# Performance work log

Hardware: AMD Instinct MI355X
Metric: run time of the kernel (lower is better)

The kernel has to match this reference:

```python
import jax, jax.numpy as jnp
import numpy as np

B, P, D, C = 1024, 4, 512, 128  # batch, parts, feat_dim, num_classes


def setup_inputs() -> dict:
    key = jax.random.key(0)
    k1, k2 = jax.random.split(key)
    # scale 0.05 keeps dot products O(1) so exp() stays in fp32 range
    inputs = jax.random.normal(k1, (B, P, D), dtype=jnp.float32) * 0.05
    targets = jax.random.randint(k2, (B,), 0, C, dtype=jnp.int64)
    return {"inputs": inputs, "targets": targets}


def _npairs_loss(inputs, targets):
    b, p, d = inputs.shape
    n = b * p
    X = inputs.reshape(n, d)
    t = jnp.repeat(targets, p)              # (n,) class label per row
    parts = jnp.tile(jnp.arange(p), b)      # (n,) part id per row
    prod = X @ X.T                          # (n, n) similarities

    sc = t[:, None] == t[None, :]           # same class
    sp = parts[:, None] == parts[None, :]   # same attention part
    s_sadc = (~sc) & sp
    s_dasc = sc & (~sp)
    s_dadc = (~sc) & (~sp)

    e_pos = jnp.exp(prod)                   # exp(neg) terms
    e_neg = jnp.exp(-prod)                  # exp(-pos) terms

    def group_loss(pos_mask, neg_mask):
        # sum_i sum_{j in pos_i} log(1 + sum_{k in neg_i} exp(prod[i,k] - prod[i,j]))
        # = sum log1p(S_i * exp(-prod[i,j])) with S_i = sum_{k in neg_i} exp(prod[i,k])
        S = jnp.sum(jnp.where(neg_mask, e_pos, 0.0), axis=1)        # (n,)
        terms = jnp.where(pos_mask, jnp.log1p(S[:, None] * e_neg), 0.0)
        return jnp.sum(terms)

    loss_sadc = group_loss(s_sadc, s_dadc)
    loss_dasc = group_loss(s_dasc, s_dadc)
    # NOTE: original returns loss_sadc twice and never uses loss_sasc (bug kept for fidelity)
    return (loss_sadc + loss_sadc + loss_dasc) / n


def reference(inputs, targets):
    return _npairs_loss(inputs, targets)
```

## Files before the change

### kernel.cpp

```cpp
#include <hip/hip_runtime.h>
#include <stdint.h>

#define GLOBAL_AS __attribute__((address_space(1)))
#define LDS_AS    __attribute__((address_space(3)))

typedef __attribute__((ext_vector_type(8))) __bf16 bf16x8;
typedef __attribute__((ext_vector_type(4))) float  f32x4;

static_assert(sizeof(bf16x8) == 16, "bf16x8 must be 16B");

constexpr int N  = 4096;
constexpr int DK = 512;


__global__ void k_convert(const float* __restrict__ X, __bf16* __restrict__ Xb,
                          const int* __restrict__ tbuf, int* __restrict__ cls) {
    if (blockIdx.x == 1024) {
        __shared__ int is64;
        const int t = threadIdx.x;
        if (t == 0) is64 = 1;
        __syncthreads();
        if (tbuf[4 * t + 1] != 0 || tbuf[4 * t + 3] != 0) is64 = 0;
        __syncthreads();
        const int f = is64;
#pragma unroll
        for (int q = 0; q < 4; ++q) {
            const int ti = 4 * t + q;
            const int v = tbuf[f ? 2 * ti : ti];
            cls[4 * ti + 0] = v; cls[4 * ti + 1] = v;
            cls[4 * ti + 2] = v; cls[4 * ti + 3] = v;
        }
        return;
    }
    int idx = blockIdx.x * blockDim.x + threadIdx.x;
    const float4* s = (const float4*)X;
    float4 a = s[2 * idx + 0];
    float4 b = s[2 * idx + 1];
    bf16x8 o;
    o[0] = (__bf16)a.x; o[1] = (__bf16)a.y; o[2] = (__bf16)a.z; o[3] = (__bf16)a.w;
    o[4] = (__bf16)b.x; o[5] = (__bf16)b.y; o[6] = (__bf16)b.z; o[7] = (__bf16)b.w;
    *(bf16x8*)(Xb + 8 * idx) = o;
}

__launch_bounds__(512, 4)
__global__ void k_main(const __bf16* __restrict__ Xb, const int* __restrict__ cls,
                       float* __restrict__ partials) {
    __shared__ __align__(16) __bf16 As[2][128 * 64];
    __shared__ __align__(16) __bf16 Bs[2][128 * 64];
    __shared__ float4 accR[4][128];
    __shared__ float4 accC[2][128];
    __shared__ int rowcls[128], colcls[128];

    const int tid  = threadIdx.x;
    const int lane = tid & 63;
    const int wid  = tid >> 6;
    const int wr   = wid >> 2;
    const int wc   = wid & 3;

    const int bid = (blockIdx.x & 7) * 66 + (blockIdx.x >> 3);
    int rt = (int)((sqrtf(8.0f * (float)bid + 1.0f) - 1.0f) * 0.5f);
    while (((rt + 1) * (rt + 2)) / 2 <= bid) ++rt;
    while ((rt * (rt + 1)) / 2 > bid) --rt;
    const int g  = bid - (rt * (rt + 1)) / 2;
    const int i0 = rt * 128;
    const int j0 = g * 128;
    const bool offdiag = (rt != g);

    if (tid < 128) {
        rowcls[tid] = cls[i0 + tid];
        colcls[tid] = cls[j0 + tid];
    }

    f32x4 acc[4][2] = {};

    const char* xb   = (const char*)Xb;
    const int   srow = tid >> 3;
    const int   skb  = ((tid & 7) ^ (srow & 7)) * 16;
    const int   ldst = wid * 1024;
    const int   rA   = lane & 15;
    const int   kgrp = lane >> 4;

#define STAGE(buf, kt)                                                                         \
    {                                                                                          \
        const size_t kb0 = (size_t)(kt) * 128;                                                 \
        char* AsB = (char*)(&As[(buf)][0]);                                                    \
        char* BsB = (char*)(&Bs[(buf)][0]);                                                    \
        _Pragma("unroll")                                                                      \
        for (int t = 0; t < 2; ++t) {                                                          \
            __builtin_amdgcn_global_load_lds(                                                  \
                (const GLOBAL_AS void*)(xb + (size_t)(i0 + t * 64 + srow) * 1024 + kb0 + skb), \
                (LDS_AS void*)(AsB + t * 8192 + ldst), 16, 0, 0);                              \
            __builtin_amdgcn_global_load_lds(                                                  \
                (const GLOBAL_AS void*)(xb + (size_t)(j0 + t * 64 + srow) * 1024 + kb0 + skb), \
                (LDS_AS void*)(BsB + t * 8192 + ldst), 16, 0, 0);                              \
        }                                                                                      \
    }

    STAGE(0, 0);
    __syncthreads();

    int cur = 0;
#pragma unroll
    for (int kt = 0; kt < DK / 64; ++kt) {
        if (kt < DK / 64 - 1) STAGE(cur ^ 1, kt + 1);
        const char* A_ = (const char*)(&As[cur][0]);
        const char* B_ = (const char*)(&Bs[cur][0]);
#pragma unroll
        for (int kk = 0; kk < 2; ++kk) {
            bf16x8 af[4];
            bf16x8 bg[2];
#pragma unroll
            for (int m = 0; m < 4; ++m) {
                const int r = wr * 64 + m * 16 + rA;
                af[m] = *(const bf16x8*)(A_ + r * 128 + (((kk * 4 + kgrp) ^ (r & 7)) * 16));
            }
#pragma unroll
            for (int n = 0; n < 2; ++n) {
                const int r = wc * 32 + n * 16 + rA;
                bg[n] = *(const bf16x8*)(B_ + r * 128 + (((kk * 4 + kgrp) ^ (r & 7)) * 16));
            }
#pragma unroll
            for (int m = 0; m < 4; ++m)
#pragma unroll
                for (int n = 0; n < 2; ++n)
                    acc[m][n] = __builtin_amdgcn_mfma_f32_16x16x32_bf16(bg[n], af[m],
                                                                        acc[m][n], 0, 0, 0);
        }
        if (kt < DK / 64 - 1) {
            __syncthreads();
            cur ^= 1;
        }
    }
#undef STAGE

    const int pi = rA & 3;
    int ci[4];
#pragma unroll
    for (int m = 0; m < 4; ++m) ci[m] = rowcls[wr * 64 + m * 16 + rA];

    float rS[4] = {0.f, 0.f, 0.f, 0.f};
    float rP[4] = {0.f, 0.f, 0.f, 0.f};
    float rE[4] = {0.f, 0.f, 0.f, 0.f};
    float rW[4] = {0.f, 0.f, 0.f, 0.f};

#pragma unroll
    for (int n = 0; n < 2; ++n) {
#pragma unroll
        for (int r = 0; r < 4; ++r) {
            const int cj = colcls[wc * 32 + n * 16 + kgrp * 4 + r];
            float cS = 0.f, cP = 0.f, cE = 0.f, cW = 0.f;
#pragma unroll
            for (int m = 0; m < 4; ++m) {
                const float p  = acc[m][n][r];
                const float ep = __expf(p);
                const bool sc = (ci[m] == cj);
                const bool sp = (pi == r);
                if (!sc && !sp) { rS[m] += ep; cS += ep; }
                const float w = (!sc && sp) ? 2.f : ((sc && !sp) ? 1.f : 0.f);
                rP[m] += w * p;  rE[m] += w * ep;  rW[m] += w;
                cP += w * p;     cE += w * ep;     cW += w;
            }
            if (offdiag) {
#pragma unroll
                for (int off = 1; off < 16; off <<= 1) {
                    cS += __shfl_xor(cS, off);
                    cP += __shfl_xor(cP, off);
                    cE += __shfl_xor(cE, off);
                    cW += __shfl_xor(cW, off);
                }
                if (rA == 0)
                    accC[wr][wc * 32 + n * 16 + kgrp * 4 + r] = make_float4(cS, cP, cE, cW);
            }
        }
    }
#pragma unroll
    for (int m = 0; m < 4; ++m) {
        float vS = rS[m], vP = rP[m], vE = rE[m], vW = rW[m];
        vS += __shfl_xor(vS, 16); vS += __shfl_xor(vS, 32);
        vP += __shfl_xor(vP, 16); vP += __shfl_xor(vP, 32);
        vE += __shfl_xor(vE, 16); vE += __shfl_xor(vE, 32);
        vW += __shfl_xor(vW, 16); vW += __shfl_xor(vW, 32);
        if (kgrp == 0) accR[wc][wr * 64 + m * 16 + rA] = make_float4(vS, vP, vE, vW);
    }

    __syncthreads();
    if (tid < 128) {
        float4 a0 = accR[0][tid], a1 = accR[1][tid], a2 = accR[2][tid], a3 = accR[3][tid];
        float4 o = make_float4(a0.x + a1.x + a2.x + a3.x, a0.y + a1.y + a2.y + a3.y,
                               a0.z + a1.z + a2.z + a3.z, a0.w + a1.w + a2.w + a3.w);
        ((float4*)partials)[(size_t)(i0 + tid) * 32 + g] = o;
        if (offdiag) {
            float4 c0 = accC[0][tid], c1 = accC[1][tid];
            float4 oc = make_float4(c0.x + c1.x, c0.y + c1.y, c0.z + c1.z, c0.w + c1.w);
            ((float4*)partials)[(size_t)(j0 + tid) * 32 + rt] = oc;
        }
    }
}

__global__ void k_rowloss(const float* __restrict__ partials, float* __restrict__ blockSums) {
    __shared__ float red[16];
    const int tid = threadIdx.x;
    const int sub = tid & 15;
    const int row = blockIdx.x * 16 + (tid >> 4);

    const float4* p = ((const float4*)partials) + (size_t)row * 32;
    float4 a = p[sub];
    float4 b = p[sub + 16];
    float S = a.x + b.x, P = a.y + b.y, E = a.z + b.z, W = a.w + b.w;
#pragma unroll
    for (int off = 1; off < 16; off <<= 1) {
        S += __shfl_xor(S, off);
        P += __shfl_xor(P, off);
        E += __shfl_xor(E, off);
        W += __shfl_xor(W, off);
    }
    if (sub == 0) red[tid >> 4] = W * logf(S) - P + E / S;
    __syncthreads();
    if (tid == 0) {
        float s = 0.f;
#pragma unroll
        for (int r = 0; r < 16; ++r) s += red[r];
        blockSums[blockIdx.x] = s;
    }
}

__global__ void k_final2(const float* __restrict__ blockSums, float* __restrict__ out) {
    const int t = threadIdx.x;
    float v = blockSums[t] + blockSums[t + 64] + blockSums[t + 128] + blockSums[t + 192];
#pragma unroll
    for (int off = 1; off < 64; off <<= 1) v += __shfl_xor(v, off);
    if (t == 0) out[0] = v / (float)N;
}

extern "C" void kernel_launch(void* const* d_in, const int* in_sizes, int n_in,
                              void* d_out, int out_size, void* d_ws, size_t ws_size,
                              hipStream_t stream) {
    const float* X = (const float*)d_in[0];
    const int*   T = (const int*)d_in[1];
    float* out = (float*)d_out;

    char* ws = (char*)d_ws;
    __bf16* Xb     = (__bf16*)ws;
    int*    cls    = (int*)(ws + (size_t)4 * 1024 * 1024);
    float*  parts  = (float*)(ws + (size_t)4 * 1024 * 1024 + 16 * 1024);
    float*  bsums  = (float*)ws;

    hipLaunchKernelGGL(k_convert, dim3(1025), dim3(256), 0, stream, X, Xb, T, cls);
    hipLaunchKernelGGL(k_main,    dim3(528),  dim3(512), 0, stream, Xb, cls, parts);
    hipLaunchKernelGGL(k_rowloss, dim3(256),  dim3(256), 0, stream, parts, bsums);
    hipLaunchKernelGGL(k_final2,  dim3(1),    dim3(64),  0, stream, bsums, out);
}
```

Measured before the change: 47.61 us.

## Use 128x64 triangular tiles with persistent work-stealing and triple-buffered LDS pipeline

Splits the lower-triangular Gram computation into finer 128x64 tiles (1056 tiles) processed by a persistent 1024-block grid. Idle blocks take more tiles through an atomic counter that k_convert initialises. The K loop now uses 3-stage LDS buffering with explicit vmcnt waits and a single barrier per step, and 256-thread blocks replace the 512-thread ones. The row-loss and final kernels are widened to read the new 96-slot partials layout and skip invalid slots. The aim is better load balance and less idle time from the tail and barriers, at the cost of atomic traffic and more partial slots to reduce.

```diff
diff --git a/kernel.cpp b/kernel.cpp
--- a/kernel.cpp
+++ b/kernel.cpp
@@ -11,14 +11,18 @@
 
 constexpr int N  = 4096;
 constexpr int DK = 512;
+constexpr int NTILE = 1056;
+constexpr int GRID_MAIN = 1024;
+constexpr int PW = 96;
 
 
 __global__ void k_convert(const float* __restrict__ X, __bf16* __restrict__ Xb,
-                          const int* __restrict__ tbuf, int* __restrict__ cls) {
+                          const int* __restrict__ tbuf, int* __restrict__ cls,
+                          int* __restrict__ ctr) {
     if (blockIdx.x == 1024) {
         __shared__ int is64;
         const int t = threadIdx.x;
-        if (t == 0) is64 = 1;
+        if (t == 0) { is64 = 1; ctr[0] = GRID_MAIN; }
         __syncthreads();
         if (tbuf[4 * t + 1] != 0 || tbuf[4 * t + 3] != 0) is64 = 0;
         __syncthreads();
@@ -42,82 +46,78 @@
     *(bf16x8*)(Xb + 8 * idx) = o;
 }
 
-__launch_bounds__(512, 4)
+__launch_bounds__(256, 4)
 __global__ void k_main(const __bf16* __restrict__ Xb, const int* __restrict__ cls,
-                       float* __restrict__ partials) {
-    __shared__ __align__(16) __bf16 As[2][128 * 64];
-    __shared__ __align__(16) __bf16 Bs[2][128 * 64];
-    __shared__ float4 accR[4][128];
-    __shared__ float4 accC[2][128];
-    __shared__ int rowcls[128], colcls[128];
+                       float* __restrict__ partials, int* __restrict__ ctr) {
+    __shared__ __align__(16) char smem[3][12288];
+    __shared__ int rowcls[128], colcls[64];
+    __shared__ int shsteal;
+    float4* accR = (float4*)&smem[0][0];
+    float4* accC = (float4*)&smem[1][0];
 
     const int tid  = threadIdx.x;
     const int lane = tid & 63;
     const int wid  = tid >> 6;
-    const int wr   = wid >> 2;
-    const int wc   = wid & 3;
-
-    const int bid = (blockIdx.x & 7) * 66 + (blockIdx.x >> 3);
-    int rt = (int)((sqrtf(8.0f * (float)bid + 1.0f) - 1.0f) * 0.5f);
-    while (((rt + 1) * (rt + 2)) / 2 <= bid) ++rt;
-    while ((rt * (rt + 1)) / 2 > bid) --rt;
-    const int g  = bid - (rt * (rt + 1)) / 2;
-    const int i0 = rt * 128;
-    const int j0 = g * 128;
-    const bool offdiag = (rt != g);
-
-    if (tid < 128) {
-        rowcls[tid] = cls[i0 + tid];
-        colcls[tid] = cls[j0 + tid];
-    }
-
-    f32x4 acc[4][2] = {};
-
-    const char* xb   = (const char*)Xb;
-    const int   srow = tid >> 3;
-    const int   skb  = ((tid & 7) ^ (srow & 7)) * 16;
-    const int   ldst = wid * 1024;
-    const int   rA   = lane & 15;
-    const int   kgrp = lane >> 4;
-
-#define STAGE(buf, kt)                                                                         \
-    {                                                                                          \
-        const size_t kb0 = (size_t)(kt) * 128;                                                 \
-        char* AsB = (char*)(&As[(buf)][0]);                                                    \
-        char* BsB = (char*)(&Bs[(buf)][0]);                                                    \
-        _Pragma("unroll")                                                                      \
-        for (int t = 0; t < 2; ++t) {                                                          \
-            __builtin_amdgcn_global_load_lds(                                                  \
-                (const GLOBAL_AS void*)(xb + (size_t)(i0 + t * 64 + srow) * 1024 + kb0 + skb), \
-                (LDS_AS void*)(AsB + t * 8192 + ldst), 16, 0, 0);                              \
-            __builtin_amdgcn_global_load_lds(                                                  \
-                (const GLOBAL_AS void*)(xb + (size_t)(j0 + t * 64 + srow) * 1024 + kb0 + skb), \
-                (LDS_AS void*)(BsB + t * 8192 + ldst), 16, 0, 0);                              \
-        }                                                                                      \
-    }
-
-    STAGE(0, 0);
-    __syncthreads();
-
-    int cur = 0;
-#pragma unroll
-    for (int kt = 0; kt < DK / 64; ++kt) {
-        if (kt < DK / 64 - 1) STAGE(cur ^ 1, kt + 1);
-        const char* A_ = (const char*)(&As[cur][0]);
-        const char* B_ = (const char*)(&Bs[cur][0]);
-#pragma unroll
-        for (int kk = 0; kk < 2; ++kk) {
-            bf16x8 af[4];
-            bf16x8 bg[2];
+    const int wr   = wid >> 1;
+    const int wc   = wid & 1;
+    const int rA   = lane & 15;
+    const int kgrp = lane >> 4;
+    const char* xb = (const char*)Xb;
+
+    int tile = (blockIdx.x & 7) * 132 + (blockIdx.x >> 3);
+
+    for (;;) {
+        int rt = (int)((sqrtf(4.0f * (float)tile + 1.0f) - 1.0f) * 0.5f);
+        while ((rt + 1) * (rt + 2) <= tile) ++rt;
+        while (rt * (rt + 1) > tile) --rt;
+        const int gc = tile - rt * (rt + 1);
+        const int i0 = rt * 128;
+        const int j0 = gc * 64;
+        const bool fullyBelow = (gc < 2 * rt);
+
+        if (tid < 128) rowcls[tid] = cls[i0 + tid];
+        else if (tid < 192) colcls[tid - 128] = cls[j0 + (tid - 128)];
+        __syncthreads();
+
+        f32x4 acc[4][2] = {};
+
+#define STAGE(bslot, kt)                                                                   \
+        {                                                                                  \
+            char* dst = &smem[(bslot)][0];                                                 \
+            const size_t kb = (size_t)(kt) * 64;                                           \
+            _Pragma("unroll")                                                              \
+            for (int q = 0; q < 3; ++q) {                                                  \
+                const int l    = q * 256 + tid;                                            \
+                const int prow = l >> 2;                                                   \
+                const int csrc = (l & 3) ^ ((prow >> 1) & 3);                              \
+                const int grow = (prow < 128) ? (i0 + prow) : (j0 + prow - 128);           \
+                __builtin_amdgcn_global_load_lds(                                          \
+                    (const GLOBAL_AS void*)(xb + (size_t)grow * 1024 + kb + csrc * 16),    \
+                    (LDS_AS void*)(dst + q * 4096 + wid * 1024), 16, 0, 0);                \
+            }                                                                              \
+        }
+
+        STAGE(0, 0);
+        STAGE(1, 1);
+
+#pragma unroll
+        for (int t = 0; t < 16; ++t) {
+            if (t < 15) { asm volatile("s_waitcnt vmcnt(3)" ::: "memory"); }
+            else        { asm volatile("s_waitcnt vmcnt(0)" ::: "memory"); }
+            __builtin_amdgcn_s_barrier();
+            asm volatile("" ::: "memory");
+            if (t + 2 < 16) STAGE((t + 2) % 3, t + 2);
+            const char* bp = &smem[t % 3][0];
+            bf16x8 af[4], bg[2];
 #pragma unroll
             for (int m = 0; m < 4; ++m) {
-                const int r = wr * 64 + m * 16 + rA;
-                af[m] = *(const bf16x8*)(A_ + r * 128 + (((kk * 4 + kgrp) ^ (r & 7)) * 16));
+                const int pr = wr * 64 + m * 16 + rA;
+                af[m] = *(const bf16x8*)(bp + pr * 64 + ((kgrp ^ ((pr >> 1) & 3)) << 4));
             }
 #pragma unroll
             for (int n = 0; n < 2; ++n) {
-                const int r = wc * 32 + n * 16 + rA;
-                bg[n] = *(const bf16x8*)(B_ + r * 128 + (((kk * 4 + kgrp) ^ (r & 7)) * 16));
+                const int pr = 128 + wc * 32 + n * 16 + rA;
+                bg[n] = *(const bf16x8*)(bp + pr * 64 + ((kgrp ^ ((pr >> 1) & 3)) << 4));
             }
 #pragma unroll
             for (int m = 0; m < 4; ++m)
@@ -126,110 +126,120 @@
                     acc[m][n] = __builtin_amdgcn_mfma_f32_16x16x32_bf16(bg[n], af[m],
                                                                         acc[m][n], 0, 0, 0);
         }
-        if (kt < DK / 64 - 1) {
-            __syncthreads();
-            cur ^= 1;
-        }
-    }
 #undef STAGE
 
-    const int pi = rA & 3;
-    int ci[4];
-#pragma unroll
-    for (int m = 0; m < 4; ++m) ci[m] = rowcls[wr * 64 + m * 16 + rA];
-
-    float rS[4] = {0.f, 0.f, 0.f, 0.f};
-    float rP[4] = {0.f, 0.f, 0.f, 0.f};
-    float rE[4] = {0.f, 0.f, 0.f, 0.f};
-    float rW[4] = {0.f, 0.f, 0.f, 0.f};
-
-#pragma unroll
-    for (int n = 0; n < 2; ++n) {
-#pragma unroll
-        for (int r = 0; r < 4; ++r) {
-            const int cj = colcls[wc * 32 + n * 16 + kgrp * 4 + r];
-            float cS = 0.f, cP = 0.f, cE = 0.f, cW = 0.f;
-#pragma unroll
-            for (int m = 0; m < 4; ++m) {
-                const float p  = acc[m][n][r];
-                const float ep = __expf(p);
-                const bool sc = (ci[m] == cj);
-                const bool sp = (pi == r);
-                if (!sc && !sp) { rS[m] += ep; cS += ep; }
-                const float w = (!sc && sp) ? 2.f : ((sc && !sp) ? 1.f : 0.f);
-                rP[m] += w * p;  rE[m] += w * ep;  rW[m] += w;
-                cP += w * p;     cE += w * ep;     cW += w;
+        __syncthreads();
+
+        const int pi = rA & 3;
+        int ci[4];
+#pragma unroll
+        for (int m = 0; m < 4; ++m) ci[m] = rowcls[wr * 64 + m * 16 + rA];
+        float rS[4] = {0.f, 0.f, 0.f, 0.f};
+        float rP[4] = {0.f, 0.f, 0.f, 0.f};
+        float rE[4] = {0.f, 0.f, 0.f, 0.f};
+        float rW[4] = {0.f, 0.f, 0.f, 0.f};
+
+#pragma unroll
+        for (int n = 0; n < 2; ++n) {
+#pragma unroll
+            for (int r = 0; r < 4; ++r) {
+                const int cj = colcls[wc * 32 + n * 16 + kgrp * 4 + r];
+                float cS = 0.f, cP = 0.f, cE = 0.f, cW = 0.f;
+#pragma unroll
+                for (int m = 0; m < 4; ++m) {
+                    const float p  = acc[m][n][r];
+                    const float ep = __expf(p);
+                    const bool sc = (ci[m] == cj);
+                    const bool sp = (pi == r);
+                    if (!sc && !sp) { rS[m] += ep; cS += ep; }
+                    const float w = (!sc && sp) ? 2.f : ((sc && !sp) ? 1.f : 0.f);
+                    rP[m] += w * p;  rE[m] += w * ep;  rW[m] += w;
+                    cP += w * p;     cE += w * ep;     cW += w;
+                }
+                if (fullyBelow) {
+#pragma unroll
+                    for (int off = 1; off < 16; off <<= 1) {
+                        cS += __shfl_xor(cS, off);
+                        cP += __shfl_xor(cP, off);
+                        cE += __shfl_xor(cE, off);
+                        cW += __shfl_xor(cW, off);
+                    }
+                    if (rA == 0)
+                        accC[wr * 64 + wc * 32 + n * 16 + kgrp * 4 + r] =
+                            make_float4(cS, cP, cE, cW);
+                }
             }
-            if (offdiag) {
-#pragma unroll
-                for (int off = 1; off < 16; off <<= 1) {
-                    cS += __shfl_xor(cS, off);
-                    cP += __shfl_xor(cP, off);
-                    cE += __shfl_xor(cE, off);
-                    cW += __shfl_xor(cW, off);
-                }
-                if (rA == 0)
-                    accC[wr][wc * 32 + n * 16 + kgrp * 4 + r] = make_float4(cS, cP, cE, cW);
-            }
-        }
-    }
-#pragma unroll
-    for (int m = 0; m < 4; ++m) {
-        float vS = rS[m], vP = rP[m], vE = rE[m], vW = rW[m];
-        vS += __shfl_xor(vS, 16); vS += __shfl_xor(vS, 32);
-        vP += __shfl_xor(vP, 16); vP += __shfl_xor(vP, 32);
-        vE += __shfl_xor(vE, 16); vE += __shfl_xor(vE, 32);
-        vW += __shfl_xor(vW, 16); vW += __shfl_xor(vW, 32);
-        if (kgrp == 0) accR[wc][wr * 64 + m * 16 + rA] = make_float4(vS, vP, vE, vW);
-    }
-
-    __syncthreads();
-    if (tid < 128) {
-        float4 a0 = accR[0][tid], a1 = accR[1][tid], a2 = accR[2][tid], a3 = accR[3][tid];
-        float4 o = make_float4(a0.x + a1.x + a2.x + a3.x, a0.y + a1.y + a2.y + a3.y,
-                               a0.z + a1.z + a2.z + a3.z, a0.w + a1.w + a2.w + a3.w);
-        ((float4*)partials)[(size_t)(i0 + tid) * 32 + g] = o;
-        if (offdiag) {
-            float4 c0 = accC[0][tid], c1 = accC[1][tid];
-            float4 oc = make_float4(c0.x + c1.x, c0.y + c1.y, c0.z + c1.z, c0.w + c1.w);
-            ((float4*)partials)[(size_t)(j0 + tid) * 32 + rt] = oc;
-        }
+        }
+#pragma unroll
+        for (int m = 0; m < 4; ++m) {
+            float vS = rS[m], vP = rP[m], vE = rE[m], vW = rW[m];
+            vS += __shfl_xor(vS, 16); vS += __shfl_xor(vS, 32);
+            vP += __shfl_xor(vP, 16); vP += __shfl_xor(vP, 32);
+            vE += __shfl_xor(vE, 16); vE += __shfl_xor(vE, 32);
+            vW += __shfl_xor(vW, 16); vW += __shfl_xor(vW, 32);
+            if (kgrp == 0) accR[wc * 128 + wr * 64 + m * 16 + rA] = make_float4(vS, vP, vE, vW);
+        }
+
+        __syncthreads();
+        if (tid < 128) {
+            float4 a0 = accR[tid], a1 = accR[128 + tid];
+            ((float4*)partials)[(size_t)(i0 + tid) * PW + gc] =
+                make_float4(a0.x + a1.x, a0.y + a1.y, a0.z + a1.z, a0.w + a1.w);
+        } else if (tid < 192 && fullyBelow) {
+            const int c = tid - 128;
+            float4 c0 = accC[c], c1 = accC[64 + c];
+            ((float4*)partials)[(size_t)(j0 + c) * PW + 64 + rt] =
+                make_float4(c0.x + c1.x, c0.y + c1.y, c0.z + c1.z, c0.w + c1.w);
+        }
+
+        if (tid == 0) shsteal = atomicAdd(ctr, 1);
+        __syncthreads();
+        const int t2 = shsteal;
+        if (t2 >= NTILE) break;
+        tile = (t2 & 7) * 132 + (t2 >> 3);
     }
 }
 
 __global__ void k_rowloss(const float* __restrict__ partials, float* __restrict__ blockSums) {
-    __shared__ float red[16];
+    __shared__ float red[4];
     const int tid = threadIdx.x;
-    const int sub = tid & 15;
-    const int row = blockIdx.x * 16 + (tid >> 4);
-
-    const float4* p = ((const float4*)partials) + (size_t)row * 32;
-    float4 a = p[sub];
-    float4 b = p[sub + 16];
-    float S = a.x + b.x, P = a.y + b.y, E = a.z + b.z, W = a.w + b.w;
-#pragma unroll
-    for (int off = 1; off < 16; off <<= 1) {
+    const int lane = tid & 63;
+    const int w = tid >> 6;
+    const int row = blockIdx.x * 4 + w;
+    const int dEnd   = 2 * (row >> 7) + 2;
+    const int mStart = ((row >> 6) + 2) >> 1;
+
+    const float4* p = (const float4*)partials + (size_t)row * PW;
+    float S = 0.f, P = 0.f, E = 0.f, W_ = 0.f;
+#pragma unroll
+    for (int s = lane; s < PW; s += 64) {
+        const bool valid = (s < 64) ? (s < dEnd) : ((s - 64) >= mStart);
+        if (valid) {
+            float4 v = p[s];
+            S += v.x; P += v.y; E += v.z; W_ += v.w;
+        }
+    }
+#pragma unroll
+    for (int off = 1; off < 64; off <<= 1) {
         S += __shfl_xor(S, off);
         P += __shfl_xor(P, off);
         E += __shfl_xor(E, off);
-        W += __shfl_xor(W, off);
-    }
-    if (sub == 0) red[tid >> 4] = W * logf(S) - P + E / S;
+        W_ += __shfl_xor(W_, off);
+    }
+    if (lane == 0) red[w] = W_ * logf(S) - P + E / S;
     __syncthreads();
-    if (tid == 0) {
-        float s = 0.f;
-#pragma unroll
-        for (int r = 0; r < 16; ++r) s += red[r];
-        blockSums[blockIdx.x] = s;
-    }
+    if (tid == 0) blockSums[blockIdx.x] = red[0] + red[1] + red[2] + red[3];
 }
 
 __global__ void k_final2(const float* __restrict__ blockSums, float* __restrict__ out) {
+    __shared__ float red[4];
     const int t = threadIdx.x;
-    float v = blockSums[t] + blockSums[t + 64] + blockSums[t + 128] + blockSums[t + 192];
+    float v = blockSums[t] + blockSums[t + 256] + blockSums[t + 512] + blockSums[t + 768];
 #pragma unroll
     for (int off = 1; off < 64; off <<= 1) v += __shfl_xor(v, off);
-    if (t == 0) out[0] = v / (float)N;
+    if ((t & 63) == 0) red[t >> 6] = v;
+    __syncthreads();
+    if (t == 0) out[0] = (red[0] + red[1] + red[2] + red[3]) / (float)N;
 }
 
 extern "C" void kernel_launch(void* const* d_in, const int* in_sizes, int n_in,
@@ -240,13 +250,14 @@
     float* out = (float*)d_out;
 
     char* ws = (char*)d_ws;
-    __bf16* Xb     = (__bf16*)ws;
-    int*    cls    = (int*)(ws + (size_t)4 * 1024 * 1024);
-    float*  parts  = (float*)(ws + (size_t)4 * 1024 * 1024 + 16 * 1024);
-    float*  bsums  = (float*)ws;
-
-    hipLaunchKernelGGL(k_convert, dim3(1025), dim3(256), 0, stream, X, Xb, T, cls);
-    hipLaunchKernelGGL(k_main,    dim3(528),  dim3(512), 0, stream, Xb, cls, parts);
-    hipLaunchKernelGGL(k_rowloss, dim3(256),  dim3(256), 0, stream, parts, bsums);
-    hipLaunchKernelGGL(k_final2,  dim3(1),    dim3(64),  0, stream, bsums, out);
-}
+    __bf16* Xb    = (__bf16*)ws;
+    int*    cls   = (int*)(ws + (size_t)4 * 1024 * 1024);
+    int*    ctr   = (int*)(ws + (size_t)4 * 1024 * 1024 + 16 * 1024);
+    float*  parts = (float*)(ws + (size_t)4 * 1024 * 1024 + 16 * 1024 + 256);
+    float*  bsums = (float*)ws;
+
+    hipLaunchKernelGGL(k_convert, dim3(1025), dim3(256), 0, stream, X, Xb, T, cls, ctr);
+    hipLaunchKernelGGL(k_main,    dim3(GRID_MAIN), dim3(256), 0, stream, Xb, cls, parts, ctr);
+    hipLaunchKernelGGL(k_rowloss, dim3(1024), dim3(256), 0, stream, parts, bsums);
+    hipLaunchKernelGGL(k_final2,  dim3(1),    dim3(256), 0, stream, bsums, out);
+}
```

New measurement: 54.62 us. +14.7%, slower.

## Drop LDS staging in tile GEMM; load MFMA fragments directly from global memory

Applied to the files above, without the earlier changes.

The main kernel no longer stages A/B tiles in LDS through double-buffered global_load_lds. Each wave now reads its bf16x8 fragments directly from global memory, relying on L1/L2 for reuse. The block shrinks from 8 to 4 waves, and each wave computes a larger 64x64 sub-tile (4x4 MFMA accumulators). This removes LDS traffic and the per-k-step barriers, but each fragment load is now a strided 16-byte global read with no explicit prefetch. It also raises register pressure and lowers the number of waves per block.

```diff
diff --git a/kernel.cpp b/kernel.cpp
--- a/kernel.cpp
+++ b/kernel.cpp
@@ -1,9 +1,6 @@
 #include <hip/hip_runtime.h>
 #include <stdint.h>
 
-#define GLOBAL_AS __attribute__((address_space(1)))
-#define LDS_AS    __attribute__((address_space(3)))
-
 typedef __attribute__((ext_vector_type(8))) __bf16 bf16x8;
 typedef __attribute__((ext_vector_type(4))) float  f32x4;
 
@@ -11,6 +8,8 @@
 
 constexpr int N  = 4096;
 constexpr int DK = 512;
+constexpr int NTILE = 528;
+constexpr int PW = 32;
 
 
 __global__ void k_convert(const float* __restrict__ X, __bf16* __restrict__ Xb,
@@ -42,20 +41,20 @@
     *(bf16x8*)(Xb + 8 * idx) = o;
 }
 
-__launch_bounds__(512, 4)
+__launch_bounds__(256, 3)
 __global__ void k_main(const __bf16* __restrict__ Xb, const int* __restrict__ cls,
                        float* __restrict__ partials) {
-    __shared__ __align__(16) __bf16 As[2][128 * 64];
-    __shared__ __align__(16) __bf16 Bs[2][128 * 64];
-    __shared__ float4 accR[4][128];
+    __shared__ float4 accR[2][128];
     __shared__ float4 accC[2][128];
     __shared__ int rowcls[128], colcls[128];
 
     const int tid  = threadIdx.x;
     const int lane = tid & 63;
     const int wid  = tid >> 6;
-    const int wr   = wid >> 2;
-    const int wc   = wid & 3;
+    const int wr   = wid >> 1;
+    const int wc   = wid & 1;
+    const int rA   = lane & 15;
+    const int kgrp = lane >> 4;
 
     const int bid = (blockIdx.x & 7) * 66 + (blockIdx.x >> 3);
     int rt = (int)((sqrtf(8.0f * (float)bid + 1.0f) - 1.0f) * 0.5f);
@@ -66,88 +65,50 @@
     const int j0 = g * 128;
     const bool offdiag = (rt != g);
 
-    if (tid < 128) {
-        rowcls[tid] = cls[i0 + tid];
-        colcls[tid] = cls[j0 + tid];
-    }
-
-    f32x4 acc[4][2] = {};
-
-    const char* xb   = (const char*)Xb;
-    const int   srow = tid >> 3;
-    const int   skb  = ((tid & 7) ^ (srow & 7)) * 16;
-    const int   ldst = wid * 1024;
-    const int   rA   = lane & 15;
-    const int   kgrp = lane >> 4;
-
-#define STAGE(buf, kt)                                                                         \
-    {                                                                                          \
-        const size_t kb0 = (size_t)(kt) * 128;                                                 \
-        char* AsB = (char*)(&As[(buf)][0]);                                                    \
-        char* BsB = (char*)(&Bs[(buf)][0]);                                                    \
-        _Pragma("unroll")                                                                      \
-        for (int t = 0; t < 2; ++t) {                                                          \
-            __builtin_amdgcn_global_load_lds(                                                  \
-                (const GLOBAL_AS void*)(xb + (size_t)(i0 + t * 64 + srow) * 1024 + kb0 + skb), \
-                (LDS_AS void*)(AsB + t * 8192 + ldst), 16, 0, 0);                              \
-            __builtin_amdgcn_global_load_lds(                                                  \
-                (const GLOBAL_AS void*)(xb + (size_t)(j0 + t * 64 + srow) * 1024 + kb0 + skb), \
-                (LDS_AS void*)(BsB + t * 8192 + ldst), 16, 0, 0);                              \
-        }                                                                                      \
-    }
-
-    STAGE(0, 0);
+    if (tid < 128) rowcls[tid] = cls[i0 + tid];
+    else           colcls[tid - 128] = cls[j0 + (tid - 128)];
     __syncthreads();
 
-    int cur = 0;
-#pragma unroll
-    for (int kt = 0; kt < DK / 64; ++kt) {
-        if (kt < DK / 64 - 1) STAGE(cur ^ 1, kt + 1);
-        const char* A_ = (const char*)(&As[cur][0]);
-        const char* B_ = (const char*)(&Bs[cur][0]);
-#pragma unroll
-        for (int kk = 0; kk < 2; ++kk) {
-            bf16x8 af[4];
-            bf16x8 bg[2];
-#pragma unroll
-            for (int m = 0; m < 4; ++m) {
-                const int r = wr * 64 + m * 16 + rA;
-                af[m] = *(const bf16x8*)(A_ + r * 128 + (((kk * 4 + kgrp) ^ (r & 7)) * 16));
-            }
-#pragma unroll
-            for (int n = 0; n < 2; ++n) {
-                const int r = wc * 32 + n * 16 + rA;
-                bg[n] = *(const bf16x8*)(B_ + r * 128 + (((kk * 4 + kgrp) ^ (r & 7)) * 16));
-            }
-#pragma unroll
-            for (int m = 0; m < 4; ++m)
-#pragma unroll
-                for (int n = 0; n < 2; ++n)
-                    acc[m][n] = __builtin_amdgcn_mfma_f32_16x16x32_bf16(bg[n], af[m],
-                                                                        acc[m][n], 0, 0, 0);
-        }
-        if (kt < DK / 64 - 1) {
-            __syncthreads();
-            cur ^= 1;
-        }
-    }
-#undef STAGE
+    const __bf16* aP[4];
+    const __bf16* bP[4];
+#pragma unroll
+    for (int m = 0; m < 4; ++m)
+        aP[m] = Xb + (size_t)(i0 + wr * 64 + m * 16 + rA) * DK + kgrp * 8;
+#pragma unroll
+    for (int n = 0; n < 4; ++n)
+        bP[n] = Xb + (size_t)(j0 + wc * 64 + n * 16 + rA) * DK + kgrp * 8;
+
+    f32x4 acc[4][4] = {};
+
+#pragma unroll
+    for (int t = 0; t < 16; ++t) {
+        bf16x8 af[4], bg[4];
+#pragma unroll
+        for (int m = 0; m < 4; ++m) af[m] = *(const bf16x8*)(aP[m] + t * 32);
+#pragma unroll
+        for (int n = 0; n < 4; ++n) bg[n] = *(const bf16x8*)(bP[n] + t * 32);
+#pragma unroll
+        for (int m = 0; m < 4; ++m)
+#pragma unroll
+            for (int n = 0; n < 4; ++n)
+                acc[m][n] = __builtin_amdgcn_mfma_f32_16x16x32_bf16(bg[n], af[m],
+                                                                    acc[m][n], 0, 0, 0);
+    }
 
     const int pi = rA & 3;
     int ci[4];
 #pragma unroll
     for (int m = 0; m < 4; ++m) ci[m] = rowcls[wr * 64 + m * 16 + rA];
-
     float rS[4] = {0.f, 0.f, 0.f, 0.f};
     float rP[4] = {0.f, 0.f, 0.f, 0.f};
     float rE[4] = {0.f, 0.f, 0.f, 0.f};
     float rW[4] = {0.f, 0.f, 0.f, 0.f};
 
 #pragma unroll
-    for (int n = 0; n < 2; ++n) {
+    for (int n = 0; n < 4; ++n) {
 #pragma unroll
         for (int r = 0; r < 4; ++r) {
-            const int cj = colcls[wc * 32 + n * 16 + kgrp * 4 + r];
+            const int cj = colcls[wc * 64 + n * 16 + kgrp * 4 + r];
             float cS = 0.f, cP = 0.f, cE = 0.f, cW = 0.f;
 #pragma unroll
             for (int m = 0; m < 4; ++m) {
@@ -169,7 +130,7 @@
                     cW += __shfl_xor(cW, off);
                 }
                 if (rA == 0)
-                    accC[wr][wc * 32 + n * 16 + kgrp * 4 + r] = make_float4(cS, cP, cE, cW);
+                    accC[wr][wc * 64 + n * 16 + kgrp * 4 + r] = make_float4(cS, cP, cE, cW);
             }
         }
     }
@@ -185,15 +146,14 @@
 
     __syncthreads();
     if (tid < 128) {
-        float4 a0 = accR[0][tid], a1 = accR[1][tid], a2 = accR[2][tid], a3 = accR[3][tid];
-        float4 o = make_float4(a0.x + a1.x + a2.x + a3.x, a0.y + a1.y + a2.y + a3.y,
-                               a0.z + a1.z + a2.z + a3.z, a0.w + a1.w + a2.w + a3.w);
-        ((float4*)partials)[(size_t)(i0 + tid) * 32 + g] = o;
-        if (offdiag) {
-            float4 c0 = accC[0][tid], c1 = accC[1][tid];
-            float4 oc = make_float4(c0.x + c1.x, c0.y + c1.y, c0.z + c1.z, c0.w + c1.w);
-            ((float4*)partials)[(size_t)(j0 + tid) * 32 + rt] = oc;
-        }
+        float4 a0 = accR[0][tid], a1 = accR[1][tid];
+        ((float4*)partials)[(size_t)(i0 + tid) * PW + g] =
+            make_float4(a0.x + a1.x, a0.y + a1.y, a0.z + a1.z, a0.w + a1.w);
+    } else if (offdiag) {
+        const int c = tid - 128;
+        float4 c0 = accC[0][c], c1 = accC[1][c];
+        ((float4*)partials)[(size_t)(j0 + c) * PW + rt] =
+            make_float4(c0.x + c1.x, c0.y + c1.y, c0.z + c1.z, c0.w + c1.w);
     }
 }
 
@@ -203,7 +163,7 @@
     const int sub = tid & 15;
     const int row = blockIdx.x * 16 + (tid >> 4);
 
-    const float4* p = ((const float4*)partials) + (size_t)row * 32;
+    const float4* p = ((const float4*)partials) + (size_t)row * PW;
     float4 a = p[sub];
     float4 b = p[sub + 16];
     float S = a.x + b.x, P = a.y + b.y, E = a.z + b.z, W = a.w + b.w;
@@ -240,13 +200,13 @@
     float* out = (float*)d_out;
 
     char* ws = (char*)d_ws;
-    __bf16* Xb     = (__bf16*)ws;
-    int*    cls    = (int*)(ws + (size_t)4 * 1024 * 1024);
-    float*  parts  = (float*)(ws + (size_t)4 * 1024 * 1024 + 16 * 1024);
-    float*  bsums  = (float*)ws;
-
-    hipLaunchKernelGGL(k_convert, dim3(1025), dim3(256), 0, stream, X, Xb, T, cls);
-    hipLaunchKernelGGL(k_main,    dim3(528),  dim3(512), 0, stream, Xb, cls, parts);
-    hipLaunchKernelGGL(k_rowloss, dim3(256),  dim3(256), 0, stream, parts, bsums);
-    hipLaunchKernelGGL(k_final2,  dim3(1),    dim3(64),  0, stream, bsums, out);
-}
+    __bf16* Xb    = (__bf16*)ws;
+    int*    cls   = (int*)(ws + (size_t)4 * 1024 * 1024);
+    float*  parts = (float*)(ws + (size_t)4 * 1024 * 1024 + 16 * 1024);
+    float*  bsums = (float*)ws;
+
+    hipLaunchKernelGGL(k_convert, dim3(1025),  dim3(256), 0, stream, X, Xb, T, cls);
+    hipLaunchKernelGGL(k_main,    dim3(NTILE), dim3(256), 0, stream, Xb, cls, parts);
+    hipLaunchKernelGGL(k_rowloss, dim3(256),   dim3(256), 0, stream, parts, bsums);
+    hipLaunchKernelGGL(k_final2,  dim3(1),     dim3(64),  0, stream, bsums, out);
+}
```

Result: slower. 91.48 us (+92.1%).

## Launch one resident wave of main-kernel blocks and hand out leftover tiles via atomic counter

Applied to the files above, without the earlier changes.

The main GEMM-plus-epilogue kernel now launches 512 blocks instead of 528 and wraps its body in a loop. Each block processes its assigned tile, then claims one of the 16 leftover triangle tiles from a global atomic counter that the convert kernel resets. This aims to avoid scheduling a second partial wave of fresh blocks and to start the tail tiles as soon as any block frees up. In exchange it adds an atomic and an extra barrier per tile, and the loop may raise register pressure.

```diff
diff --git a/kernel.cpp b/kernel.cpp
--- a/kernel.cpp
+++ b/kernel.cpp
@@ -11,14 +11,17 @@
 
 constexpr int N  = 4096;
 constexpr int DK = 512;
+constexpr int NTILE = 528;
+constexpr int GRID_MAIN = 512;
 
 
 __global__ void k_convert(const float* __restrict__ X, __bf16* __restrict__ Xb,
-                          const int* __restrict__ tbuf, int* __restrict__ cls) {
+                          const int* __restrict__ tbuf, int* __restrict__ cls,
+                          int* __restrict__ ctr) {
     if (blockIdx.x == 1024) {
         __shared__ int is64;
         const int t = threadIdx.x;
-        if (t == 0) is64 = 1;
+        if (t == 0) { is64 = 1; ctr[0] = GRID_MAIN; }
         __syncthreads();
         if (tbuf[4 * t + 1] != 0 || tbuf[4 * t + 3] != 0) is64 = 0;
         __syncthreads();
@@ -44,156 +47,166 @@
 
 __launch_bounds__(512, 4)
 __global__ void k_main(const __bf16* __restrict__ Xb, const int* __restrict__ cls,
-                       float* __restrict__ partials) {
+                       float* __restrict__ partials, int* __restrict__ ctr) {
     __shared__ __align__(16) __bf16 As[2][128 * 64];
     __shared__ __align__(16) __bf16 Bs[2][128 * 64];
     __shared__ float4 accR[4][128];
     __shared__ float4 accC[2][128];
     __shared__ int rowcls[128], colcls[128];
+    __shared__ int shsteal;
 
     const int tid  = threadIdx.x;
     const int lane = tid & 63;
     const int wid  = tid >> 6;
     const int wr   = wid >> 2;
     const int wc   = wid & 3;
-
-    const int bid = (blockIdx.x & 7) * 66 + (blockIdx.x >> 3);
-    int rt = (int)((sqrtf(8.0f * (float)bid + 1.0f) - 1.0f) * 0.5f);
-    while (((rt + 1) * (rt + 2)) / 2 <= bid) ++rt;
-    while ((rt * (rt + 1)) / 2 > bid) --rt;
-    const int g  = bid - (rt * (rt + 1)) / 2;
-    const int i0 = rt * 128;
-    const int j0 = g * 128;
-    const bool offdiag = (rt != g);
-
-    if (tid < 128) {
-        rowcls[tid] = cls[i0 + tid];
-        colcls[tid] = cls[j0 + tid];
-    }
-
-    f32x4 acc[4][2] = {};
+    const int rA   = lane & 15;
+    const int kgrp = lane >> 4;
 
     const char* xb   = (const char*)Xb;
     const int   srow = tid >> 3;
     const int   skb  = ((tid & 7) ^ (srow & 7)) * 16;
     const int   ldst = wid * 1024;
-    const int   rA   = lane & 15;
-    const int   kgrp = lane >> 4;
+
+    int tile = (blockIdx.x & 7) * 66 + (blockIdx.x >> 3);
+
+    for (;;) {
+        int rt = (int)((sqrtf(8.0f * (float)tile + 1.0f) - 1.0f) * 0.5f);
+        while (((rt + 1) * (rt + 2)) / 2 <= tile) ++rt;
+        while ((rt * (rt + 1)) / 2 > tile) --rt;
+        const int g  = tile - (rt * (rt + 1)) / 2;
+        const int i0 = rt * 128;
+        const int j0 = g * 128;
+        const bool offdiag = (rt != g);
+
+        if (tid < 128) {
+            rowcls[tid] = cls[i0 + tid];
+            colcls[tid] = cls[j0 + tid];
+        }
 
 #define STAGE(buf, kt)                                                                         \
-    {                                                                                          \
-        const size_t kb0 = (size_t)(kt) * 128;                                                 \
-        char* AsB = (char*)(&As[(buf)][0]);                                                    \
-        char* BsB = (char*)(&Bs[(buf)][0]);                                                    \
-        _Pragma("unroll")                                                                      \
-        for (int t = 0; t < 2; ++t) {                                                          \
-            __builtin_amdgcn_global_load_lds(                                                  \
-                (const GLOBAL_AS void*)(xb + (size_t)(i0 + t * 64 + srow) * 1024 + kb0 + skb), \
-                (LDS_AS void*)(AsB + t * 8192 + ldst), 16, 0, 0);                              \
-            __builtin_amdgcn_global_load_lds(                                                  \
-                (const GLOBAL_AS void*)(xb + (size_t)(j0 + t * 64 + srow) * 1024 + kb0 + skb), \
-                (LDS_AS void*)(BsB + t * 8192 + ldst), 16, 0, 0);                              \
-        }                                                                                      \
-    }
-
-    STAGE(0, 0);
-    __syncthreads();
-
-    int cur = 0;
-#pragma unroll
-    for (int kt = 0; kt < DK / 64; ++kt) {
-        if (kt < DK / 64 - 1) STAGE(cur ^ 1, kt + 1);
-        const char* A_ = (const char*)(&As[cur][0]);
-        const char* B_ = (const char*)(&Bs[cur][0]);
-#pragma unroll
-        for (int kk = 0; kk < 2; ++kk) {
-            bf16x8 af[4];
-            bf16x8 bg[2];
-#pragma unroll
-            for (int m = 0; m < 4; ++m) {
-                const int r = wr * 64 + m * 16 + rA;
-                af[m] = *(const bf16x8*)(A_ + r * 128 + (((kk * 4 + kgrp) ^ (r & 7)) * 16));
-            }
-#pragma unroll
-            for (int n = 0; n < 2; ++n) {
-                const int r = wc * 32 + n * 16 + rA;
-                bg[n] = *(const bf16x8*)(B_ + r * 128 + (((kk * 4 + kgrp) ^ (r & 7)) * 16));
-            }
-#pragma unroll
-            for (int m = 0; m < 4; ++m)
-#pragma unroll
-                for (int n = 0; n < 2; ++n)
-                    acc[m][n] = __builtin_amdgcn_mfma_f32_16x16x32_bf16(bg[n], af[m],
-                                                                        acc[m][n], 0, 0, 0);
-        }
-        if (kt < DK / 64 - 1) {
-            __syncthreads();
-            cur ^= 1;
-        }
-    }
+        {                                                                                      \
+            const size_t kb0 = (size_t)(kt) * 128;                                             \
+            char* AsB = (char*)(&As[(buf)][0]);                                                \
+            char* BsB = (char*)(&Bs[(buf)][0]);                                                \
+            _Pragma("unroll")                                                                  \
+            for (int t = 0; t < 2; ++t) {                                                      \
+                __builtin_amdgcn_global_load_lds(                                              \
+                    (const GLOBAL_AS void*)(xb + (size_t)(i0 + t * 64 + srow) * 1024 + kb0 + skb), \
+                    (LDS_AS void*)(AsB + t * 8192 + ldst), 16, 0, 0);                          \
+                __builtin_amdgcn_global_load_lds(                                              \
+                    (const GLOBAL_AS void*)(xb + (size_t)(j0 + t * 64 + srow) * 1024 + kb0 + skb), \
+                    (LDS_AS void*)(BsB + t * 8192 + ldst), 16, 0, 0);                          \
+            }                                                                                  \
+        }
+
+        STAGE(0, 0);
+        __syncthreads();
+
+        f32x4 acc[4][2] = {};
+        int cur = 0;
+#pragma unroll
+        for (int kt = 0; kt < DK / 64; ++kt) {
+            if (kt < DK / 64 - 1) STAGE(cur ^ 1, kt + 1);
+            const char* A_ = (const char*)(&As[cur][0]);
+            const char* B_ = (const char*)(&Bs[cur][0]);
+#pragma unroll
+            for (int kk = 0; kk < 2; ++kk) {
+                bf16x8 af[4];
+                bf16x8 bg[2];
+#pragma unroll
+                for (int m = 0; m < 4; ++m) {
+                    const int r = wr * 64 + m * 16 + rA;
+                    af[m] = *(const bf16x8*)(A_ + r * 128 + (((kk * 4 + kgrp) ^ (r & 7)) * 16));
+                }
+#pragma unroll
+                for (int n = 0; n < 2; ++n) {
+                    const int r = wc * 32 + n * 16 + rA;
+                    bg[n] = *(const bf16x8*)(B_ + r * 128 + (((kk * 4 + kgrp) ^ (r & 7)) * 16));
+                }
+#pragma unroll
+                for (int m = 0; m < 4; ++m)
+#pragma unroll
+                    for (int n = 0; n < 2; ++n)
+                        acc[m][n] = __builtin_amdgcn_mfma_f32_16x16x32_bf16(bg[n], af[m],
+                                                                            acc[m][n], 0, 0, 0);
+            }
+            if (kt < DK / 64 - 1) {
+                __syncthreads();
+                cur ^= 1;
+            }
+        }
 #undef STAGE
 
-    const int pi = rA & 3;
-    int ci[4];
-#pragma unroll
-    for (int m = 0; m < 4; ++m) ci[m] = rowcls[wr * 64 + m * 16 + rA];
-
-    float rS[4] = {0.f, 0.f, 0.f, 0.f};
-    float rP[4] = {0.f, 0.f, 0.f, 0.f};
-    float rE[4] = {0.f, 0.f, 0.f, 0.f};
-    float rW[4] = {0.f, 0.f, 0.f, 0.f};
-
-#pragma unroll
-    for (int n = 0; n < 2; ++n) {
-#pragma unroll
-        for (int r = 0; r < 4; ++r) {
-            const int cj = colcls[wc * 32 + n * 16 + kgrp * 4 + r];
-            float cS = 0.f, cP = 0.f, cE = 0.f, cW = 0.f;
-#pragma unroll
-            for (int m = 0; m < 4; ++m) {
-                const float p  = acc[m][n][r];
-                const float ep = __expf(p);
-                const bool sc = (ci[m] == cj);
-                const bool sp = (pi == r);
-                if (!sc && !sp) { rS[m] += ep; cS += ep; }
-                const float w = (!sc && sp) ? 2.f : ((sc && !sp) ? 1.f : 0.f);
-                rP[m] += w * p;  rE[m] += w * ep;  rW[m] += w;
-                cP += w * p;     cE += w * ep;     cW += w;
-            }
+        const int pi = rA & 3;
+        int ci[4];
+#pragma unroll
+        for (int m = 0; m < 4; ++m) ci[m] = rowcls[wr * 64 + m * 16 + rA];
+
+        float rS[4] = {0.f, 0.f, 0.f, 0.f};
+        float rP[4] = {0.f, 0.f, 0.f, 0.f};
+        float rE[4] = {0.f, 0.f, 0.f, 0.f};
+        float rW[4] = {0.f, 0.f, 0.f, 0.f};
+
+#pragma unroll
+        for (int n = 0; n < 2; ++n) {
+#pragma unroll
+            for (int r = 0; r < 4; ++r) {
+                const int cj = colcls[wc * 32 + n * 16 + kgrp * 4 + r];
+                float cS = 0.f, cP = 0.f, cE = 0.f, cW = 0.f;
+#pragma unroll
+                for (int m = 0; m < 4; ++m) {
+                    const float p  = acc[m][n][r];
+                    const float ep = __expf(p);
+                    const bool sc = (ci[m] == cj);
+                    const bool sp = (pi == r);
+                    if (!sc && !sp) { rS[m] += ep; cS += ep; }
+                    const float w = (!sc && sp) ? 2.f : ((sc && !sp) ? 1.f : 0.f);
+                    rP[m] += w * p;  rE[m] += w * ep;  rW[m] += w;
+                    cP += w * p;     cE += w * ep;     cW += w;
+                }
+                if (offdiag) {
+#pragma unroll
+                    for (int off = 1; off < 16; off <<= 1) {
+                        cS += __shfl_xor(cS, off);
+                        cP += __shfl_xor(cP, off);
+                        cE += __shfl_xor(cE, off);
+                        cW += __shfl_xor(cW, off);
+                    }
+                    if (rA == 0)
+                        accC[wr][wc * 32 + n * 16 + kgrp * 4 + r] = make_float4(cS, cP, cE, cW);
+                }
+            }
+        }
+#pragma unroll
+        for (int m = 0; m < 4; ++m) {
+            float vS = rS[m], vP = rP[m], vE = rE[m], vW = rW[m];
+            vS += __shfl_xor(vS, 16); vS += __shfl_xor(vS, 32);
+            vP += __shfl_xor(vP, 16); vP += __shfl_xor(vP, 32);
+            vE += __shfl_xor(vE, 16); vE += __shfl_xor(vE, 32);
+            vW += __shfl_xor(vW, 16); vW += __shfl_xor(vW, 32);
+            if (kgrp == 0) accR[wc][wr * 64 + m * 16 + rA] = make_float4(vS, vP, vE, vW);
+        }
+
+        __syncthreads();
+        if (tid < 128) {
+            float4 a0 = accR[0][tid], a1 = accR[1][tid], a2 = accR[2][tid], a3 = accR[3][tid];
+            float4 o = make_float4(a0.x + a1.x + a2.x + a3.x, a0.y + a1.y + a2.y + a3.y,
+                                   a0.z + a1.z + a2.z + a3.z, a0.w + a1.w + a2.w + a3.w);
+            ((float4*)partials)[(size_t)(i0 + tid) * 32 + g] = o;
             if (offdiag) {
-#pragma unroll
-                for (int off = 1; off < 16; off <<= 1) {
-                    cS += __shfl_xor(cS, off);
-                    cP += __shfl_xor(cP, off);
-                    cE += __shfl_xor(cE, off);
-                    cW += __shfl_xor(cW, off);
-                }
-                if (rA == 0)
-                    accC[wr][wc * 32 + n * 16 + kgrp * 4 + r] = make_float4(cS, cP, cE, cW);
-            }
-        }
-    }
-#pragma unroll
-    for (int m = 0; m < 4; ++m) {
-        float vS = rS[m], vP = rP[m], vE = rE[m], vW = rW[m];
-        vS += __shfl_xor(vS, 16); vS += __shfl_xor(vS, 32);
-        vP += __shfl_xor(vP, 16); vP += __shfl_xor(vP, 32);
-        vE += __shfl_xor(vE, 16); vE += __shfl_xor(vE, 32);
-        vW += __shfl_xor(vW, 16); vW += __shfl_xor(vW, 32);
-        if (kgrp == 0) accR[wc][wr * 64 + m * 16 + rA] = make_float4(vS, vP, vE, vW);
-    }
-
-    __syncthreads();
-    if (tid < 128) {
-        float4 a0 = accR[0][tid], a1 = accR[1][tid], a2 = accR[2][tid], a3 = accR[3][tid];
-        float4 o = make_float4(a0.x + a1.x + a2.x + a3.x, a0.y + a1.y + a2.y + a3.y,
-                               a0.z + a1.z + a2.z + a3.z, a0.w + a1.w + a2.w + a3.w);
-        ((float4*)partials)[(size_t)(i0 + tid) * 32 + g] = o;
-        if (offdiag) {
-            float4 c0 = accC[0][tid], c1 = accC[1][tid];
-            float4 oc = make_float4(c0.x + c1.x, c0.y + c1.y, c0.z + c1.z, c0.w + c1.w);
-            ((float4*)partials)[(size_t)(j0 + tid) * 32 + rt] = oc;
-        }
+                float4 c0 = accC[0][tid], c1 = accC[1][tid];
+                float4 oc = make_float4(c0.x + c1.x, c0.y + c1.y, c0.z + c1.z, c0.w + c1.w);
+                ((float4*)partials)[(size_t)(j0 + tid) * 32 + rt] = oc;
+            }
+        }
+
+        if (tid == 0) shsteal = atomicAdd(ctr, 1);
+        __syncthreads();
+        const int t2 = shsteal;
+        if (t2 >= NTILE) break;
+        const int e = t2 - GRID_MAIN;
+        tile = (e >> 1) * 66 + 64 + (e & 1);
     }
 }
 
@@ -240,13 +253,14 @@
     float* out = (float*)d_out;
 
     char* ws = (char*)d_ws;
-    __bf16* Xb     = (__bf16*)ws;
-    int*    cls    = (int*)(ws + (size_t)4 * 1024 * 1024);
-    float*  parts  = (float*)(ws + (size_t)4 * 1024 * 1024 + 16 * 1024);
-    float*  bsums  = (float*)ws;
-
-    hipLaunchKernelGGL(k_convert, dim3(1025), dim3(256), 0, stream, X, Xb, T, cls);
-    hipLaunchKernelGGL(k_main,    dim3(528),  dim3(512), 0, stream, Xb, cls, parts);
-    hipLaunchKernelGGL(k_rowloss, dim3(256),  dim3(256), 0, stream, parts, bsums);
-    hipLaunchKernelGGL(k_final2,  dim3(1),    dim3(64),  0, stream, bsums, out);
-}
+    __bf16* Xb    = (__bf16*)ws;
+    int*    cls   = (int*)(ws + (size_t)4 * 1024 * 1024);
+    int*    ctr   = (int*)(ws + (size_t)4 * 1024 * 1024 + 16 * 1024);
+    float*  parts = (float*)(ws + (size_t)4 * 1024 * 1024 + 16 * 1024 + 256);
+    float*  bsums = (float*)ws;
+
+    hipLaunchKernelGGL(k_convert, dim3(1025),      dim3(256), 0, stream, X, Xb, T, cls, ctr);
+    hipLaunchKernelGGL(k_main,    dim3(GRID_MAIN), dim3(512), 0, stream, Xb, cls, parts, ctr);
+    hipLaunchKernelGGL(k_rowloss, dim3(256),       dim3(256), 0, stream, parts, bsums);
+    hipLaunchKernelGGL(k_final2,  dim3(1),         dim3(64),  0, stream, bsums, out);
+}
```

After: 53.21 us. 11.8% more time.
